# Kernel optimization log

Measured on AMD Instinct MI355X. Metric: run time of the kernel, lower is better.

The kernel has to match this reference:

```python
import jax, jax.numpy as jnp
import numpy as np

B, S, D_MODEL, N_HEADS, D_K, D_V = 2, 2048, 1024, 16, 64, 64


def setup_inputs() -> dict:
    key = jax.random.key(0)
    ks = jax.random.split(key, 11)
    s_in = 1.0 / np.sqrt(D_MODEL)
    s_out = 1.0 / np.sqrt(N_HEADS * D_V)
    return {
        "Q": jax.random.normal(ks[0], (B, S, D_MODEL), jnp.float32),
        "K": jax.random.normal(ks[1], (B, S, D_MODEL), jnp.float32),
        "V": jax.random.normal(ks[2], (B, S, D_MODEL), jnp.float32),
        # per-head projection weights (stacked over heads), Linear-style: y = x @ W + b
        "Wq": jax.random.uniform(ks[3], (N_HEADS, D_MODEL, D_K), jnp.float32, -s_in, s_in),
        "bq": jax.random.uniform(ks[4], (N_HEADS, D_K), jnp.float32, -s_in, s_in),
        "Wk": jax.random.uniform(ks[5], (N_HEADS, D_MODEL, D_K), jnp.float32, -s_in, s_in),
        "bk": jax.random.uniform(ks[6], (N_HEADS, D_K), jnp.float32, -s_in, s_in),
        "Wv": jax.random.uniform(ks[7], (N_HEADS, D_MODEL, D_V), jnp.float32, -s_in, s_in),
        "bv": jax.random.uniform(ks[8], (N_HEADS, D_V), jnp.float32, -s_in, s_in),
        "Wo": jax.random.uniform(ks[9], (N_HEADS * D_V, D_MODEL), jnp.float32, -s_out, s_out),
        "bo": jax.random.uniform(ks[10], (D_MODEL,), jnp.float32, -s_out, s_out),
    }


def reference(Q, K, V, Wq, bq, Wk, bk, Wv, bv, Wo, bo):
    # Per-head projections, batched over heads: [B,H,S,dk/dv]
    QW = jnp.einsum("bsd,hdk->bhsk", Q, Wq) + bq[None, :, None, :]
    KW = jnp.einsum("bsd,hdk->bhsk", K, Wk) + bk[None, :, None, :]
    VW = jnp.einsum("bsd,hdv->bhsv", V, Wv) + bv[None, :, None, :]
    scores = jnp.einsum("bhsk,bhtk->bhst", QW, KW)  # [B,H,S,S]
    # Faithful to torch source: softmax(scores)/d_k**1/2 == softmax(scores)/(2*d_k)
    attn = jax.nn.softmax(scores, axis=-1) * (1.0 / (2.0 * D_K))
    heads = jnp.einsum("bhst,bhtv->bhsv", attn, VW)  # [B,H,S,dv]
    # concat heads along feature dim -> [B,S,H*dv], then output projection
    concat = heads.transpose(0, 2, 1, 3).reshape(B, S, N_HEADS * D_V)
    return concat @ Wo + bo
```

## Files before the change

kernel.cpp:

```cpp
#include <hip/hip_runtime.h>

#define BB 2
#define SS 2048
#define DM 1024
#define HH 16
#define DK 64
#define LOG2E 1.44269504088896340736f

typedef __attribute__((ext_vector_type(8))) short short8;
typedef __attribute__((ext_vector_type(4))) float f32x4;
typedef __attribute__((ext_vector_type(16))) float f32x16;

#define MFMA16(a, b, c) __builtin_amdgcn_mfma_f32_16x16x32_bf16(a, b, c, 0, 0, 0)
#define MFMA32(a, b, c) __builtin_amdgcn_mfma_f32_32x32x16_bf16(a, b, c, 0, 0, 0)

#if __has_builtin(__builtin_amdgcn_exp2f)
#define EXP2(x) __builtin_amdgcn_exp2f(x)
#else
#define EXP2(x) __expf((x) * 0.6931471805599453f)
#endif

#define WAITV(N) asm volatile("s_waitcnt vmcnt(" #N ")" ::: "memory")
#define BAR() __builtin_amdgcn_s_barrier()

static __device__ __forceinline__ unsigned short f2bf(float f) {
    unsigned u = __builtin_bit_cast(unsigned, f);
    u += 0x7fffu + ((u >> 16) & 1u);
    return (unsigned short)(u >> 16);
}
static __device__ __forceinline__ float bf2f(unsigned short u) {
    return __builtin_bit_cast(float, ((unsigned)u) << 16);
}

static __device__ __forceinline__ void gld16(const void* g, void* l) {
    __builtin_amdgcn_global_load_lds(
        (const __attribute__((address_space(1))) unsigned int*)g,
        (__attribute__((address_space(3))) unsigned int*)l, 16, 0, 0);
}

__global__ __launch_bounds__(256) void cvt3_kernel(
    const float* __restrict__ p0, const float* __restrict__ p1,
    const float* __restrict__ p2, unsigned short* __restrict__ o0,
    unsigned short* __restrict__ o1, unsigned short* __restrict__ o2) {
    const int m = blockIdx.y;
    const float* in = m == 0 ? p0 : (m == 1 ? p1 : p2);
    unsigned short* out = m == 0 ? o0 : (m == 1 ? o1 : o2);
    const int i = (blockIdx.x * 256 + threadIdx.x) * 8;
    float4 a = *(const float4*)(in + i);
    float4 b = *(const float4*)(in + i + 4);
    union { unsigned short u[8]; uint4 v; } x;
    x.u[0] = f2bf(a.x); x.u[1] = f2bf(a.y); x.u[2] = f2bf(a.z); x.u[3] = f2bf(a.w);
    x.u[4] = f2bf(b.x); x.u[5] = f2bf(b.y); x.u[6] = f2bf(b.z); x.u[7] = f2bf(b.w);
    *(uint4*)(out + i) = x.v;
}

__global__ __launch_bounds__(256) void wtrans4_kernel(
    const float* __restrict__ Wq, const float* __restrict__ Wk,
    const float* __restrict__ Wv, const float* __restrict__ Wo,
    unsigned short* __restrict__ Wqt, unsigned short* __restrict__ Wkt,
    unsigned short* __restrict__ Wvt, unsigned short* __restrict__ Wot) {
    __shared__ float t[64][65];
    const int which = blockIdx.y;
    const float* in;
    unsigned short* out;
    int r0, c0, C;
    if (which < 3) {
        in = which == 0 ? Wq : (which == 1 ? Wk : Wv);
        out = which == 0 ? Wqt : (which == 1 ? Wkt : Wvt);
        const int h = blockIdx.x >> 4;
        r0 = (blockIdx.x & 15) * 64; c0 = 0; C = DK;
        in += (size_t)h * DM * DK;
        out += (size_t)h * DK * DM;
    } else {
        in = Wo; out = Wot;
        r0 = (blockIdx.x & 15) * 64; c0 = (blockIdx.x >> 4) * 64; C = DM;
    }
    const int lr = threadIdx.x & 63, gg = threadIdx.x >> 6;
    #pragma unroll
    for (int p = 0; p < 16; ++p) {
        const int r = p * 4 + gg;
        t[r][lr] = in[(size_t)(r0 + r) * C + c0 + lr];
    }
    __syncthreads();
    #pragma unroll
    for (int p = 0; p < 16; ++p) {
        const int c = p * 4 + gg;
        out[(size_t)(c0 + c) * DM + r0 + lr] = f2bf(t[lr][c]);
    }
}

#define GSTAGE(Ap, Btp, k0, pp)                                              \
    do {                                                                     \
        _Pragma("unroll")                                                    \
        for (int i = 0; i < 4; ++i) {                                        \
            const int idx = tid + i * 256;                                   \
            const int row = idx >> 3, c8 = (idx & 7) * 8;                    \
            gld16(&Ap[(size_t)(r0 + row) * DM + (k0) + c8], &As[pp][idx * 8]); \
            gld16(&Btp[(size_t)(n0 + row) * DM + (k0) + c8], &Bs[pp][idx * 8]); \
        }                                                                    \
    } while (0)

#define GCOMPUTE(pp)                                                         \
    do {                                                                     \
        _Pragma("unroll")                                                    \
        for (int kc = 0; kc < 2; ++kc) {                                     \
            short8 a[4], b[4];                                               \
            _Pragma("unroll")                                                \
            for (int i = 0; i < 4; ++i) {                                    \
                a[i] = *(const short8*)&As[pp][(wr + i * 16 + lr) * 64 + kc * 32 + lg * 8]; \
                b[i] = *(const short8*)&Bs[pp][(wc + i * 16 + lr) * 64 + kc * 32 + lg * 8]; \
            }                                                                \
            __builtin_amdgcn_s_setprio(1);                                   \
            _Pragma("unroll")                                                \
            for (int mi = 0; mi < 4; ++mi)                                   \
                _Pragma("unroll")                                            \
                for (int ni = 0; ni < 4; ++ni)                               \
                    acc[mi][ni] = MFMA16(a[mi], b[ni], acc[mi][ni]);         \
            __builtin_amdgcn_s_setprio(0);                                   \
        }                                                                    \
    } while (0)

#define GEMM_MAIN(Ap, Btp)                                                   \
    GSTAGE(Ap, Btp, 0, 0);                                                   \
    for (int k = 0; k < 14 * 64; k += 128) {                                 \
        GSTAGE(Ap, Btp, k + 64, 1);                                          \
        WAITV(8); BAR();                                                     \
        GCOMPUTE(0);                                                         \
        BAR();                                                               \
        GSTAGE(Ap, Btp, k + 128, 0);                                         \
        WAITV(8); BAR();                                                     \
        GCOMPUTE(1);                                                         \
        BAR();                                                               \
    }                                                                        \
    GSTAGE(Ap, Btp, 15 * 64, 1);                                             \
    WAITV(8); BAR();                                                         \
    GCOMPUTE(0);                                                             \
    BAR();                                                                   \
    WAITV(0); BAR();                                                         \
    GCOMPUTE(1);

__global__ __launch_bounds__(256) void qkv_gemm_kernel(
    const unsigned short* __restrict__ Qb, const unsigned short* __restrict__ Kb,
    const unsigned short* __restrict__ Vb,
    const unsigned short* __restrict__ Wqt, const unsigned short* __restrict__ Wkt,
    const unsigned short* __restrict__ Wvt,
    const float* __restrict__ bq, const float* __restrict__ bk,
    const float* __restrict__ bv,
    unsigned short* __restrict__ QWp, unsigned short* __restrict__ KWp,
    unsigned short* __restrict__ VWt) {
    __shared__ unsigned short As[2][128 * 64];
    __shared__ unsigned short Bs[2][128 * 64];
    const int z = blockIdx.z;
    const unsigned short* A  = z == 0 ? Qb : (z == 1 ? Kb : Vb);
    const unsigned short* Bt = z == 0 ? Wqt : (z == 1 ? Wkt : Wvt);
    const float* bias = z == 0 ? bq : (z == 1 ? bk : bv);
    const int tid = threadIdx.x;
    const int r0 = blockIdx.x * 128, n0 = blockIdx.y * 128;
    const int w = tid >> 6, lane = tid & 63, lr = lane & 15, lg = lane >> 4;
    const int wr = (w >> 1) * 64, wc = (w & 1) * 64;

    const f32x4 zf = {0.f, 0.f, 0.f, 0.f};
    f32x4 acc[4][4];
    #pragma unroll
    for (int mi = 0; mi < 4; ++mi)
        #pragma unroll
        for (int ni = 0; ni < 4; ++ni) acc[mi][ni] = zf;

    GEMM_MAIN(A, Bt);

    const float scale = (z == 0) ? LOG2E : 1.0f;
    #pragma unroll
    for (int ni = 0; ni < 4; ++ni) {
        const int col = n0 + wc + ni * 16 + lr;
        const float bb = bias[col];
        #pragma unroll
        for (int mi = 0; mi < 4; ++mi) {
            const int rbase = r0 + wr + mi * 16 + lg * 4;
            const f32x4 v = acc[mi][ni];
            if (z == 2) {
                const int b = rbase >> 11, s = rbase & (SS - 1);
                const int h = col >> 6, vv = col & 63;
                union { unsigned short u[4]; unsigned long long q; } x;
                #pragma unroll
                for (int j = 0; j < 4; ++j) x.u[j] = f2bf(v[j] + bb);
                *(unsigned long long*)&VWt[((size_t)(b * HH + h) * 64 + vv) * SS + s] = x.q;
            } else {
                unsigned short* C = z == 0 ? QWp : KWp;
                #pragma unroll
                for (int j = 0; j < 4; ++j)
                    C[(size_t)(rbase + j) * DM + col] = f2bf((v[j] + bb) * scale);
            }
        }
    }
}

__global__ __launch_bounds__(256) void outproj_kernel(
    const unsigned short* __restrict__ A, const unsigned short* __restrict__ Bt,
    const float* __restrict__ bias, float* __restrict__ Cout) {
    __shared__ unsigned short As[2][128 * 64];
    __shared__ unsigned short Bs[2][128 * 64];
    const int tid = threadIdx.x;
    const int r0 = blockIdx.x * 128, n0 = blockIdx.y * 128;
    const int w = tid >> 6, lane = tid & 63, lr = lane & 15, lg = lane >> 4;
    const int wr = (w >> 1) * 64, wc = (w & 1) * 64;

    const f32x4 zf = {0.f, 0.f, 0.f, 0.f};
    f32x4 acc[4][4];
    #pragma unroll
    for (int mi = 0; mi < 4; ++mi)
        #pragma unroll
        for (int ni = 0; ni < 4; ++ni) acc[mi][ni] = zf;

    GEMM_MAIN(A, Bt);

    #pragma unroll
    for (int ni = 0; ni < 4; ++ni) {
        const int col = n0 + wc + ni * 16 + lr;
        const float bb = bias[col];
        #pragma unroll
        for (int mi = 0; mi < 4; ++mi) {
            const int rbase = r0 + wr + mi * 16 + lg * 4;
            const f32x4 v = acc[mi][ni];
            #pragma unroll
            for (int j = 0; j < 4; ++j)
                Cout[(size_t)(rbase + j) * DM + col] = v[j] + bb;
        }
    }
}

#define FRAG(buf, row, col) \
    (*(const short8*)&buf[(row) * 64 + ((col) ^ (((row) & 7) << 3))])

__global__ __launch_bounds__(256, 2) void attn_kernel(
    const unsigned short* __restrict__ QW,
    const unsigned short* __restrict__ KW,
    const unsigned short* __restrict__ VWt,
    unsigned short* __restrict__ CC) {
    __shared__ unsigned short Ks[3][64 * 64];
    __shared__ unsigned short Vs[3][64 * 64];
    const int tid = threadIdx.x;
    const int w = tid >> 6, lane = tid & 63;
    const int ql = lane & 31, hi = lane >> 5, hi8 = hi * 8;

    const int wgid = blockIdx.x;
    const int kk = wgid >> 3;
    const int bh = (kk >> 4) * 8 + (wgid & 7);
    const int b = bh >> 4, h = bh & 15;
    const int row0 = (kk & 15) * 128;
    const int q = row0 + w * 32 + ql;

    short8 qf[4];
    const unsigned short* Qp = QW + ((size_t)b * SS + q) * DM + h * DK;
    #pragma unroll
    for (int kc = 0; kc < 4; ++kc)
        qf[kc] = *(const short8*)(Qp + kc * 16 + hi8);

    const unsigned short* Kp = KW + (size_t)b * SS * DM + h * DK;
    const unsigned short* Vt = VWt + (size_t)bh * 64 * SS;

    const int sidx0 = tid, sidx1 = tid + 256;
    const int srow0 = sidx0 >> 3, sc0 = ((sidx0 & 7) ^ (srow0 & 7)) * 8;
    const int srow1 = sidx1 >> 3, sc1 = ((sidx1 & 7) ^ (srow1 & 7)) * 8;

#define STAGE(t0, pp)                                                        \
    do {                                                                     \
        gld16(&Kp[(size_t)((t0) + srow0) * DM + sc0], &Ks[pp][sidx0 * 8]);   \
        gld16(&Vt[(size_t)srow0 * SS + (t0) + sc0], &Vs[pp][sidx0 * 8]);     \
        gld16(&Kp[(size_t)((t0) + srow1) * DM + sc1], &Ks[pp][sidx1 * 8]);   \
        gld16(&Vt[(size_t)srow1 * SS + (t0) + sc1], &Vs[pp][sidx1 * 8]);     \
    } while (0)

    const f32x16 z16 = {0.f};
    const short8 ones = {(short)0x3F80, (short)0x3F80, (short)0x3F80, (short)0x3F80,
                         (short)0x3F80, (short)0x3F80, (short)0x3F80, (short)0x3F80};
    f32x16 o0 = z16, o1 = z16, lv = z16;
    f32x16 sA0, sA1, sB0, sB1;

#define QKT(bQ, sd0, sd1)                                                        \
    do {                                                                         \
        __builtin_amdgcn_s_setprio(1);                                           \
        sd0 = MFMA32(FRAG(Ks[bQ], ql, hi8), qf[0], z16);                         \
        sd1 = MFMA32(FRAG(Ks[bQ], 32 + ql, hi8), qf[0], z16);                    \
        _Pragma("unroll")                                                        \
        for (int kc = 1; kc < 4; ++kc) {                                         \
            sd0 = MFMA32(FRAG(Ks[bQ], ql, kc * 16 + hi8), qf[kc], sd0);          \
            sd1 = MFMA32(FRAG(Ks[bQ], 32 + ql, kc * 16 + hi8), qf[kc], sd1);     \
        }                                                                        \
        __builtin_amdgcn_s_setprio(0);                                           \
    } while (0)

#define PACK2(sx, pa0, pa1)                                                      \
    do {                                                                         \
        unsigned x, x2, y, y2, u, u2, v, v2;                                     \
        asm("v_cvt_pk_bf16_f32 %0, %1, %2" : "=v"(x)  : "v"(sx[0]), "v"(sx[1])); \
        asm("v_cvt_pk_bf16_f32 %0, %1, %2" : "=v"(x2) : "v"(sx[2]), "v"(sx[3])); \
        asm("v_cvt_pk_bf16_f32 %0, %1, %2" : "=v"(y)  : "v"(sx[4]), "v"(sx[5])); \
        asm("v_cvt_pk_bf16_f32 %0, %1, %2" : "=v"(y2) : "v"(sx[6]), "v"(sx[7])); \
        asm("v_cvt_pk_bf16_f32 %0, %1, %2" : "=v"(u)  : "v"(sx[8]), "v"(sx[9])); \
        asm("v_cvt_pk_bf16_f32 %0, %1, %2" : "=v"(u2) : "v"(sx[10]), "v"(sx[11])); \
        asm("v_cvt_pk_bf16_f32 %0, %1, %2" : "=v"(v)  : "v"(sx[12]), "v"(sx[13])); \
        asm("v_cvt_pk_bf16_f32 %0, %1, %2" : "=v"(v2) : "v"(sx[14]), "v"(sx[15])); \
        asm("v_permlane32_swap_b32 %0, %1" : "+v"(x),  "+v"(y));                 \
        asm("v_permlane32_swap_b32 %0, %1" : "+v"(x2), "+v"(y2));                \
        asm("v_permlane32_swap_b32 %0, %1" : "+v"(u),  "+v"(v));                 \
        asm("v_permlane32_swap_b32 %0, %1" : "+v"(u2), "+v"(v2));                \
        union { unsigned uu[4]; short8 s8; } k0, k1;                             \
        k0.uu[0] = x; k0.uu[1] = x2; k0.uu[2] = y; k0.uu[3] = y2;                \
        k1.uu[0] = u; k1.uu[1] = u2; k1.uu[2] = v; k1.uu[3] = v2;                \
        pa0 = k0.s8; pa1 = k1.s8;                                                \
    } while (0)

#define PVT(bP, sx0, sx1)                                                        \
    do {                                                                         \
        _Pragma("unroll")                                                        \
        for (int r = 0; r < 16; ++r) sx0[r] = EXP2(sx0[r]);                      \
        short8 pa0, pa1, pa2, pa3;                                               \
        PACK2(sx0, pa0, pa1);                                                    \
        __builtin_amdgcn_s_setprio(1);                                           \
        o0 = MFMA32(FRAG(Vs[bP], ql, hi8), pa0, o0);                             \
        lv = MFMA32(ones, pa0, lv);                                              \
        o1 = MFMA32(FRAG(Vs[bP], 32 + ql, hi8), pa0, o1);                        \
        o0 = MFMA32(FRAG(Vs[bP], ql, 16 + hi8), pa1, o0);                        \
        lv = MFMA32(ones, pa1, lv);                                              \
        o1 = MFMA32(FRAG(Vs[bP], 32 + ql, 16 + hi8), pa1, o1);                   \
        __builtin_amdgcn_s_setprio(0);                                           \
        _Pragma("unroll")                                                        \
        for (int r = 0; r < 16; ++r) sx1[r] = EXP2(sx1[r]);                      \
        PACK2(sx1, pa2, pa3);                                                    \
        __builtin_amdgcn_s_setprio(1);                                           \
        o0 = MFMA32(FRAG(Vs[bP], ql, 32 + hi8), pa2, o0);                        \
        lv = MFMA32(ones, pa2, lv);                                              \
        o1 = MFMA32(FRAG(Vs[bP], 32 + ql, 32 + hi8), pa2, o1);                   \
        o0 = MFMA32(FRAG(Vs[bP], ql, 48 + hi8), pa3, o0);                        \
        lv = MFMA32(ones, pa3, lv);                                              \
        o1 = MFMA32(FRAG(Vs[bP], 32 + ql, 48 + hi8), pa3, o1);                   \
        __builtin_amdgcn_s_setprio(0);                                           \
    } while (0)

#define SUBT(t, bS, bQ, bP, si0, si1, so0, so1)                              \
    do {                                                                     \
        STAGE(((t) + 2) * 64, bS);                                           \
        WAITV(4); BAR();                                                     \
        QKT(bQ, so0, so1);                                                   \
        PVT(bP, si0, si1);                                                   \
        BAR();                                                               \
    } while (0)

    STAGE(0, 0);
    WAITV(0); BAR();
    QKT(0, sA0, sA1);
    STAGE(64, 1);

    for (int tt = 0; tt < 30; tt += 6) {
        SUBT(tt + 0, 2, 1, 0, sA0, sA1, sB0, sB1);
        SUBT(tt + 1, 0, 2, 1, sB0, sB1, sA0, sA1);
        SUBT(tt + 2, 1, 0, 2, sA0, sA1, sB0, sB1);
        SUBT(tt + 3, 2, 1, 0, sB0, sB1, sA0, sA1);
        SUBT(tt + 4, 0, 2, 1, sA0, sA1, sB0, sB1);
        SUBT(tt + 5, 1, 0, 2, sB0, sB1, sA0, sA1);
    }

    WAITV(0); BAR();
    QKT(1, sB0, sB1);
    PVT(0, sA0, sA1);
    PVT(1, sB0, sB1);
#undef STAGE
#undef SUBT

    const float inv = 1.0f / (lv[0] * 128.0f);
    unsigned short* cp = CC + ((size_t)b * SS + q) * DM + h * DK;
    #pragma unroll
    for (int vt = 0; vt < 2; ++vt) {
        const f32x16 ov = vt ? o1 : o0;
        #pragma unroll
        for (int m2 = 0; m2 < 4; ++m2) {
            union { unsigned short u[4]; unsigned long long q8; } pk;
            #pragma unroll
            for (int c = 0; c < 4; ++c) pk.u[c] = f2bf(ov[m2 * 4 + c] * inv);
            *(unsigned long long*)(cp + vt * 32 + m2 * 8 + hi * 4) = pk.q8;
        }
    }
}

extern "C" void kernel_launch(void* const* d_in, const int* in_sizes, int n_in,
                              void* d_out, int out_size, void* d_ws, size_t ws_size,
                              hipStream_t stream) {
    const float* Q  = (const float*)d_in[0];
    const float* K  = (const float*)d_in[1];
    const float* V  = (const float*)d_in[2];
    const float* Wq = (const float*)d_in[3];
    const float* bq = (const float*)d_in[4];
    const float* Wk = (const float*)d_in[5];
    const float* bk = (const float*)d_in[6];
    const float* Wv = (const float*)d_in[7];
    const float* bv = (const float*)d_in[8];
    const float* Wo = (const float*)d_in[9];
    const float* bo = (const float*)d_in[10];
    float* out = (float*)d_out;

    unsigned short* ws = (unsigned short*)d_ws;
    const size_t MK = (size_t)BB * SS * DM;
    const size_t WK = (size_t)DM * DM;
    unsigned short* Qb  = ws;
    unsigned short* Kb  = Qb + MK;
    unsigned short* Vb  = Kb + MK;
    unsigned short* Wqt = Vb + MK;
    unsigned short* Wkt = Wqt + WK;
    unsigned short* Wvt = Wkt + WK;
    unsigned short* Wot = Wvt + WK;
    unsigned short* QWp = Wot + WK;
    unsigned short* KWp = QWp + MK;
    unsigned short* VWt = KWp + MK;
    unsigned short* CCp = Qb;

    dim3 blk(256);
    const int M = BB * SS;

    hipLaunchKernelGGL(cvt3_kernel, dim3(MK / 2048, 3), blk, 0, stream,
                       Q, K, V, Qb, Kb, Vb);

    hipLaunchKernelGGL(wtrans4_kernel, dim3(256, 4), blk, 0, stream,
                       Wq, Wk, Wv, Wo, Wqt, Wkt, Wvt, Wot);

    hipLaunchKernelGGL(qkv_gemm_kernel, dim3(M / 128, 8, 3), blk, 0, stream,
                       Qb, Kb, Vb, Wqt, Wkt, Wvt, bq, bk, bv, QWp, KWp, VWt);

    hipLaunchKernelGGL(attn_kernel, dim3(512), blk, 0, stream,
                       QWp, KWp, VWt, CCp);

    hipLaunchKernelGGL(outproj_kernel, dim3(M / 128, 8), blk, 0, stream,
                       CCp, Wot, bo, out);
}
```

Baseline: 127.2 us.

## Fuse fp32-to-bf16 input conversion into QKV GEMM and retile out-projection

Removes the separate conversion kernel: the QKV GEMM now loads fp32 activations into registers, converts them to bf16 with v_cvt_pk_bf16_f32, and writes them to padded LDS while the next tile's loads are in flight. The K-tile shrinks from 64 to 32 and the weight tiles get an XOR-swizzled LDS layout. The out-projection switches to 128x64 tiles with K=32 stages, which doubles its grid for more parallelism. This saves a kernel launch and a full round trip of the bf16 copies of Q, K and V through memory. In exchange the GEMMs run more barrier-synchronised stages and the fp32 A loads go through registers instead of direct-to-LDS copies.

```diff
diff --git a/kernel.cpp b/kernel.cpp
--- a/kernel.cpp
+++ b/kernel.cpp
@@ -21,6 +21,7 @@
 #endif
 
 #define WAITV(N) asm volatile("s_waitcnt vmcnt(" #N ")" ::: "memory")
+#define LGKM0() asm volatile("s_waitcnt lgkmcnt(0)" ::: "memory")
 #define BAR() __builtin_amdgcn_s_barrier()
 
 static __device__ __forceinline__ unsigned short f2bf(float f) {
@@ -28,30 +29,11 @@
     u += 0x7fffu + ((u >> 16) & 1u);
     return (unsigned short)(u >> 16);
 }
-static __device__ __forceinline__ float bf2f(unsigned short u) {
-    return __builtin_bit_cast(float, ((unsigned)u) << 16);
-}
 
 static __device__ __forceinline__ void gld16(const void* g, void* l) {
     __builtin_amdgcn_global_load_lds(
         (const __attribute__((address_space(1))) unsigned int*)g,
         (__attribute__((address_space(3))) unsigned int*)l, 16, 0, 0);
-}
-
-__global__ __launch_bounds__(256) void cvt3_kernel(
-    const float* __restrict__ p0, const float* __restrict__ p1,
-    const float* __restrict__ p2, unsigned short* __restrict__ o0,
-    unsigned short* __restrict__ o1, unsigned short* __restrict__ o2) {
-    const int m = blockIdx.y;
-    const float* in = m == 0 ? p0 : (m == 1 ? p1 : p2);
-    unsigned short* out = m == 0 ? o0 : (m == 1 ? o1 : o2);
-    const int i = (blockIdx.x * 256 + threadIdx.x) * 8;
-    float4 a = *(const float4*)(in + i);
-    float4 b = *(const float4*)(in + i + 4);
-    union { unsigned short u[8]; uint4 v; } x;
-    x.u[0] = f2bf(a.x); x.u[1] = f2bf(a.y); x.u[2] = f2bf(a.z); x.u[3] = f2bf(a.w);
-    x.u[4] = f2bf(b.x); x.u[5] = f2bf(b.y); x.u[6] = f2bf(b.z); x.u[7] = f2bf(b.w);
-    *(uint4*)(out + i) = x.v;
 }
 
 __global__ __launch_bounds__(256) void wtrans4_kernel(
@@ -89,69 +71,19 @@
     }
 }
 
-#define GSTAGE(Ap, Btp, k0, pp)                                              \
-    do {                                                                     \
-        _Pragma("unroll")                                                    \
-        for (int i = 0; i < 4; ++i) {                                        \
-            const int idx = tid + i * 256;                                   \
-            const int row = idx >> 3, c8 = (idx & 7) * 8;                    \
-            gld16(&Ap[(size_t)(r0 + row) * DM + (k0) + c8], &As[pp][idx * 8]); \
-            gld16(&Btp[(size_t)(n0 + row) * DM + (k0) + c8], &Bs[pp][idx * 8]); \
-        }                                                                    \
-    } while (0)
-
-#define GCOMPUTE(pp)                                                         \
-    do {                                                                     \
-        _Pragma("unroll")                                                    \
-        for (int kc = 0; kc < 2; ++kc) {                                     \
-            short8 a[4], b[4];                                               \
-            _Pragma("unroll")                                                \
-            for (int i = 0; i < 4; ++i) {                                    \
-                a[i] = *(const short8*)&As[pp][(wr + i * 16 + lr) * 64 + kc * 32 + lg * 8]; \
-                b[i] = *(const short8*)&Bs[pp][(wc + i * 16 + lr) * 64 + kc * 32 + lg * 8]; \
-            }                                                                \
-            __builtin_amdgcn_s_setprio(1);                                   \
-            _Pragma("unroll")                                                \
-            for (int mi = 0; mi < 4; ++mi)                                   \
-                _Pragma("unroll")                                            \
-                for (int ni = 0; ni < 4; ++ni)                               \
-                    acc[mi][ni] = MFMA16(a[mi], b[ni], acc[mi][ni]);         \
-            __builtin_amdgcn_s_setprio(0);                                   \
-        }                                                                    \
-    } while (0)
-
-#define GEMM_MAIN(Ap, Btp)                                                   \
-    GSTAGE(Ap, Btp, 0, 0);                                                   \
-    for (int k = 0; k < 14 * 64; k += 128) {                                 \
-        GSTAGE(Ap, Btp, k + 64, 1);                                          \
-        WAITV(8); BAR();                                                     \
-        GCOMPUTE(0);                                                         \
-        BAR();                                                               \
-        GSTAGE(Ap, Btp, k + 128, 0);                                         \
-        WAITV(8); BAR();                                                     \
-        GCOMPUTE(1);                                                         \
-        BAR();                                                               \
-    }                                                                        \
-    GSTAGE(Ap, Btp, 15 * 64, 1);                                             \
-    WAITV(8); BAR();                                                         \
-    GCOMPUTE(0);                                                             \
-    BAR();                                                                   \
-    WAITV(0); BAR();                                                         \
-    GCOMPUTE(1);
-
 __global__ __launch_bounds__(256) void qkv_gemm_kernel(
-    const unsigned short* __restrict__ Qb, const unsigned short* __restrict__ Kb,
-    const unsigned short* __restrict__ Vb,
+    const float* __restrict__ Qf, const float* __restrict__ Kf,
+    const float* __restrict__ Vf,
     const unsigned short* __restrict__ Wqt, const unsigned short* __restrict__ Wkt,
     const unsigned short* __restrict__ Wvt,
     const float* __restrict__ bq, const float* __restrict__ bk,
     const float* __restrict__ bv,
     unsigned short* __restrict__ QWp, unsigned short* __restrict__ KWp,
     unsigned short* __restrict__ VWt) {
-    __shared__ unsigned short As[2][128 * 64];
-    __shared__ unsigned short Bs[2][128 * 64];
+    __shared__ unsigned short As[2][128 * 40];
+    __shared__ unsigned short Bs[2][128 * 32];
     const int z = blockIdx.z;
-    const unsigned short* A  = z == 0 ? Qb : (z == 1 ? Kb : Vb);
+    const float* A = z == 0 ? Qf : (z == 1 ? Kf : Vf);
     const unsigned short* Bt = z == 0 ? Wqt : (z == 1 ? Wkt : Wvt);
     const float* bias = z == 0 ? bq : (z == 1 ? bk : bv);
     const int tid = threadIdx.x;
@@ -166,7 +98,93 @@
         #pragma unroll
         for (int ni = 0; ni < 4; ++ni) acc[mi][ni] = zf;
 
-    GEMM_MAIN(A, Bt);
+    float4 rA[4], rB[4];
+
+#define ALOAD(k0, rr)                                                        \
+    do {                                                                     \
+        _Pragma("unroll")                                                    \
+        for (int i = 0; i < 4; ++i) {                                        \
+            const int qi = tid + i * 256;                                    \
+            const int row = qi >> 3, cc = (qi & 7) * 4;                      \
+            rr[i] = *(const float4*)&A[(size_t)(r0 + row) * DM + (k0) + cc]; \
+        }                                                                    \
+    } while (0)
+
+#define AWRITE(rr, pp)                                                       \
+    do {                                                                     \
+        _Pragma("unroll")                                                    \
+        for (int i = 0; i < 4; ++i) {                                        \
+            const int qi = tid + i * 256;                                    \
+            const int row = qi >> 3, cc = (qi & 7) * 4;                      \
+            unsigned lo, hi2;                                                \
+            asm("v_cvt_pk_bf16_f32 %0, %1, %2" : "=v"(lo)                    \
+                : "v"(rr[i].x), "v"(rr[i].y));                               \
+            asm("v_cvt_pk_bf16_f32 %0, %1, %2" : "=v"(hi2)                   \
+                : "v"(rr[i].z), "v"(rr[i].w));                               \
+            const unsigned long long v8 =                                    \
+                ((unsigned long long)hi2 << 32) | lo;                        \
+            *(unsigned long long*)&As[pp][row * 40 + cc] = v8;               \
+        }                                                                    \
+    } while (0)
+
+#define BGLD(k0, pp)                                                         \
+    do {                                                                     \
+        _Pragma("unroll")                                                    \
+        for (int i = 0; i < 2; ++i) {                                        \
+            const int idx = tid + i * 256;                                   \
+            const int row = idx >> 2;                                        \
+            const int cg = ((idx & 3) ^ (row & 3)) * 8;                      \
+            gld16(&Bt[(size_t)(n0 + row) * DM + (k0) + cg], &Bs[pp][idx * 8]); \
+        }                                                                    \
+    } while (0)
+
+#define GCOMP(pp)                                                            \
+    do {                                                                     \
+        short8 a[4], b[4];                                                   \
+        _Pragma("unroll")                                                    \
+        for (int i = 0; i < 4; ++i) {                                        \
+            a[i] = *(const short8*)&As[pp][(wr + i * 16 + lr) * 40 + lg * 8]; \
+            b[i] = *(const short8*)&Bs[pp][(wc + i * 16 + lr) * 32 +         \
+                                           ((lg * 8) ^ ((lr & 3) << 3))];    \
+        }                                                                    \
+        __builtin_amdgcn_s_setprio(1);                                       \
+        _Pragma("unroll")                                                    \
+        for (int mi = 0; mi < 4; ++mi)                                       \
+            _Pragma("unroll")                                                \
+            for (int ni = 0; ni < 4; ++ni)                                   \
+                acc[mi][ni] = MFMA16(a[mi], b[ni], acc[mi][ni]);             \
+        __builtin_amdgcn_s_setprio(0);                                       \
+    } while (0)
+
+#define QITER(cb, rcur, nb, rnxt, tn)                                        \
+    do {                                                                     \
+        ALOAD((tn) * 32, rnxt);                                              \
+        BGLD((tn) * 32, nb);                                                 \
+        WAITV(6);                                                            \
+        AWRITE(rcur, cb);                                                    \
+        LGKM0();                                                             \
+        BAR();                                                               \
+        GCOMP(cb);                                                           \
+        BAR();                                                               \
+    } while (0)
+
+    ALOAD(0, rA);
+    BGLD(0, 0);
+    for (int t = 0; t < 30; t += 2) {
+        QITER(0, rA, 1, rB, t + 1);
+        QITER(1, rB, 0, rA, t + 2);
+    }
+    QITER(0, rA, 1, rB, 31);
+    WAITV(0);
+    AWRITE(rB, 1);
+    LGKM0();
+    BAR();
+    GCOMP(1);
+#undef ALOAD
+#undef AWRITE
+#undef BGLD
+#undef GCOMP
+#undef QITER
 
     const float scale = (z == 0) ? LOG2E : 1.0f;
     #pragma unroll
@@ -197,29 +215,82 @@
 __global__ __launch_bounds__(256) void outproj_kernel(
     const unsigned short* __restrict__ A, const unsigned short* __restrict__ Bt,
     const float* __restrict__ bias, float* __restrict__ Cout) {
-    __shared__ unsigned short As[2][128 * 64];
-    __shared__ unsigned short Bs[2][128 * 64];
+    __shared__ unsigned short As[2][128 * 32];
+    __shared__ unsigned short Bs[2][64 * 32];
     const int tid = threadIdx.x;
-    const int r0 = blockIdx.x * 128, n0 = blockIdx.y * 128;
+    const int r0 = blockIdx.x * 128, n0 = blockIdx.y * 64;
     const int w = tid >> 6, lane = tid & 63, lr = lane & 15, lg = lane >> 4;
-    const int wr = (w >> 1) * 64, wc = (w & 1) * 64;
 
     const f32x4 zf = {0.f, 0.f, 0.f, 0.f};
-    f32x4 acc[4][4];
-    #pragma unroll
-    for (int mi = 0; mi < 4; ++mi)
+    f32x4 acc[2][4];
+    #pragma unroll
+    for (int mi = 0; mi < 2; ++mi)
         #pragma unroll
         for (int ni = 0; ni < 4; ++ni) acc[mi][ni] = zf;
 
-    GEMM_MAIN(A, Bt);
+#define OSTAGE(k0, pp)                                                       \
+    do {                                                                     \
+        _Pragma("unroll")                                                    \
+        for (int i = 0; i < 2; ++i) {                                        \
+            const int idx = tid + i * 256;                                   \
+            const int row = idx >> 2;                                        \
+            const int cg = ((idx & 3) ^ (row & 3)) * 8;                      \
+            gld16(&A[(size_t)(r0 + row) * DM + (k0) + cg], &As[pp][idx * 8]); \
+        }                                                                    \
+        {                                                                    \
+            const int row = tid >> 2;                                        \
+            const int cg = ((tid & 3) ^ (row & 3)) * 8;                      \
+            gld16(&Bt[(size_t)(n0 + row) * DM + (k0) + cg], &Bs[pp][tid * 8]); \
+        }                                                                    \
+    } while (0)
+
+#define OCOMP(pp)                                                            \
+    do {                                                                     \
+        short8 a[2], b[4];                                                   \
+        _Pragma("unroll")                                                    \
+        for (int i = 0; i < 2; ++i)                                          \
+            a[i] = *(const short8*)&As[pp][(w * 32 + i * 16 + lr) * 32 +     \
+                                           ((lg * 8) ^ ((lr & 3) << 3))];    \
+        _Pragma("unroll")                                                    \
+        for (int i = 0; i < 4; ++i)                                          \
+            b[i] = *(const short8*)&Bs[pp][(i * 16 + lr) * 32 +              \
+                                           ((lg * 8) ^ ((lr & 3) << 3))];    \
+        __builtin_amdgcn_s_setprio(1);                                       \
+        _Pragma("unroll")                                                    \
+        for (int mi = 0; mi < 2; ++mi)                                       \
+            _Pragma("unroll")                                                \
+            for (int ni = 0; ni < 4; ++ni)                                   \
+                acc[mi][ni] = MFMA16(a[mi], b[ni], acc[mi][ni]);             \
+        __builtin_amdgcn_s_setprio(0);                                       \
+    } while (0)
+
+    OSTAGE(0, 0);
+    for (int t = 0; t < 30; t += 2) {
+        OSTAGE((t + 1) * 32, 1);
+        WAITV(3); BAR();
+        OCOMP(0);
+        BAR();
+        OSTAGE((t + 2) * 32, 0);
+        WAITV(3); BAR();
+        OCOMP(1);
+        BAR();
+    }
+    OSTAGE(31 * 32, 1);
+    WAITV(3); BAR();
+    OCOMP(0);
+    BAR();
+    WAITV(0); BAR();
+    OCOMP(1);
+#undef OSTAGE
+#undef OCOMP
 
     #pragma unroll
     for (int ni = 0; ni < 4; ++ni) {
-        const int col = n0 + wc + ni * 16 + lr;
+        const int col = n0 + ni * 16 + lr;
         const float bb = bias[col];
         #pragma unroll
-        for (int mi = 0; mi < 4; ++mi) {
-            const int rbase = r0 + wr + mi * 16 + lg * 4;
+        for (int mi = 0; mi < 2; ++mi) {
+            const int rbase = r0 + w * 32 + mi * 16 + lg * 4;
             const f32x4 v = acc[mi][ni];
             #pragma unroll
             for (int j = 0; j < 4; ++j)
@@ -401,33 +472,27 @@
     unsigned short* ws = (unsigned short*)d_ws;
     const size_t MK = (size_t)BB * SS * DM;
     const size_t WK = (size_t)DM * DM;
-    unsigned short* Qb  = ws;
-    unsigned short* Kb  = Qb + MK;
-    unsigned short* Vb  = Kb + MK;
-    unsigned short* Wqt = Vb + MK;
+    unsigned short* Wqt = ws;
     unsigned short* Wkt = Wqt + WK;
     unsigned short* Wvt = Wkt + WK;
     unsigned short* Wot = Wvt + WK;
     unsigned short* QWp = Wot + WK;
     unsigned short* KWp = QWp + MK;
     unsigned short* VWt = KWp + MK;
-    unsigned short* CCp = Qb;
+    unsigned short* CCp = VWt + MK;
 
     dim3 blk(256);
     const int M = BB * SS;
 
-    hipLaunchKernelGGL(cvt3_kernel, dim3(MK / 2048, 3), blk, 0, stream,
-                       Q, K, V, Qb, Kb, Vb);
-
     hipLaunchKernelGGL(wtrans4_kernel, dim3(256, 4), blk, 0, stream,
                        Wq, Wk, Wv, Wo, Wqt, Wkt, Wvt, Wot);
 
     hipLaunchKernelGGL(qkv_gemm_kernel, dim3(M / 128, 8, 3), blk, 0, stream,
-                       Qb, Kb, Vb, Wqt, Wkt, Wvt, bq, bk, bv, QWp, KWp, VWt);
+                       Q, K, V, Wqt, Wkt, Wvt, bq, bk, bv, QWp, KWp, VWt);
 
     hipLaunchKernelGGL(attn_kernel, dim3(512), blk, 0, stream,
                        QWp, KWp, VWt, CCp);
 
-    hipLaunchKernelGGL(outproj_kernel, dim3(M / 128, 8), blk, 0, stream,
+    hipLaunchKernelGGL(outproj_kernel, dim3(M / 128, DM / 64), blk, 0, stream,
                        CCp, Wot, bo, out);
 }
```

Result: slower. 165.4 us (+30.0%).
